# Optimization experiments

Measured on AMD Instinct MI355X. Metric: run time of the kernel, lower is better.

The kernel has to match this reference:

```python
import jax, jax.numpy as jnp
import numpy as np

IMG_SHAPE = (256, 256, 256)


def _rot3(a):
    # Rx @ Ry @ Rz, matching _compute_rotation
    ax, ay, az = a[0], a[1], a[2]
    cx, sx = jnp.cos(ax), jnp.sin(ax)
    cy, sy = jnp.cos(ay), jnp.sin(ay)
    cz, sz = jnp.cos(az), jnp.sin(az)
    one = jnp.ones_like(ax)
    zero = jnp.zeros_like(ax)
    Rx = jnp.stack([jnp.stack([one, zero, zero]),
                    jnp.stack([zero, cx, -sx]),
                    jnp.stack([zero, sx, cx])])
    Ry = jnp.stack([jnp.stack([cy, zero, sy]),
                    jnp.stack([zero, one, zero]),
                    jnp.stack([-sy, zero, cy])])
    Rz = jnp.stack([jnp.stack([cz, -sz, zero]),
                    jnp.stack([sz, cz, zero]),
                    jnp.stack([zero, zero, one])])
    return Rx @ Ry @ Rz


def _rigid4(a, t, cog):
    # T_center_inv @ T_trans @ T_rot @ T_center
    R = _rot3(a)
    Tc = jnp.eye(4, dtype=a.dtype).at[:3, 3].set(-cog)
    Tci = jnp.eye(4, dtype=a.dtype).at[:3, 3].set(cog)
    Tt = jnp.eye(4, dtype=a.dtype).at[:3, 3].set(t)
    Tr = jnp.eye(4, dtype=a.dtype).at[:3, :3].set(R)
    return Tci @ Tt @ Tr @ Tc


def _trilinear(vol, di, dj, dk):
    # fast_3D_interp_torch(mode='linear'): trilinear interp, zero outside bounds
    D, H, W = vol.shape
    ok = (di >= 0) & (di <= D - 1) & (dj >= 0) & (dj <= H - 1) & (dk >= 0) & (dk <= W - 1)
    di = jnp.clip(di, 0.0, D - 1)
    dj = jnp.clip(dj, 0.0, H - 1)
    dk = jnp.clip(dk, 0.0, W - 1)
    fi = jnp.floor(di).astype(jnp.int32)
    fj = jnp.floor(dj).astype(jnp.int32)
    fk = jnp.floor(dk).astype(jnp.int32)
    ci = jnp.clip(fi + 1, 0, D - 1)
    cj = jnp.clip(fj + 1, 0, H - 1)
    ck = jnp.clip(fk + 1, 0, W - 1)
    wi = di - fi
    wj = dj - fj
    wk = dk - fk
    out = (vol[fi, fj, fk] * (1 - wi) * (1 - wj) * (1 - wk)
           + vol[fi, fj, ck] * (1 - wi) * (1 - wj) * wk
           + vol[fi, cj, fk] * (1 - wi) * wj * (1 - wk)
           + vol[fi, cj, ck] * (1 - wi) * wj * wk
           + vol[ci, fj, fk] * wi * (1 - wj) * (1 - wk)
           + vol[ci, fj, ck] * wi * (1 - wj) * wk
           + vol[ci, cj, fk] * wi * wj * (1 - wk)
           + vol[ci, cj, ck] * wi * wj * wk)
    return jnp.where(ok, out, jnp.zeros_like(out))


def setup_inputs() -> dict:
    key = jax.random.key(0)
    k1, k2 = jax.random.split(key)
    image_targ = jax.random.normal(k1, (1, 1) + IMG_SHAPE, dtype=jnp.float32)
    # small rotation so most of the warped grid stays in bounds (angle_factor=1)
    angle = 0.1 * jax.random.normal(k2, (1, 3), dtype=jnp.float32)
    translation = jnp.zeros((1, 3), dtype=jnp.float32)
    v2r = np.eye(4, dtype=np.float32)
    v2r[:3, 3] = -127.5  # center-of-volume RAS origin
    ref_v2r = jnp.asarray(v2r)
    flo_v2r = jnp.asarray(v2r)
    cog = jnp.zeros((3,), dtype=jnp.float32)
    return {"image_targ": image_targ, "angle": angle, "translation": translation,
            "ref_v2r": ref_v2r, "flo_v2r": flo_v2r, "cog": cog}


def reference(image_targ, angle, translation, ref_v2r, flo_v2r, cog):
    # tx_factor = angle_factor = 1 -> params used as-is
    T_rig = jax.vmap(lambda a, t: _rigid4(a, t, cog))(angle, translation)  # [B,4,4]
    T = (jnp.linalg.inv(flo_v2r) @ T_rig[0] @ ref_v2r).astype(jnp.float32)
    D, H, W = image_targ.shape[2:]
    gi, gj, gk = jnp.meshgrid(jnp.arange(D, dtype=jnp.float32),
                              jnp.arange(H, dtype=jnp.float32),
                              jnp.arange(W, dtype=jnp.float32), indexing='ij')
    di = T[0, 0] * gi + T[0, 1] * gj + T[0, 2] * gk + T[0, 3]
    dj = T[1, 0] * gi + T[1, 1] * gj + T[1, 2] * gk + T[1, 3]
    dk = T[2, 0] * gi + T[2, 1] * gj + T[2, 2] * gk + T[2, 3]
    image_reg = _trilinear(image_targ[0, 0], di, dj, dk)
    return image_reg[None, None]
```

## Files before the change

### kernel.cpp

```cpp
#include <hip/hip_runtime.h>
#include <math.h>

#define DD 256
#define HH 256
#define WW 256
#define TI 16
#define TJ 8
#define TK 16
#define LDSF 8192

typedef float f2v __attribute__((ext_vector_type(2)));
typedef f2v __attribute__((aligned(4))) f2u;
typedef float f4v __attribute__((ext_vector_type(4)));
typedef f4v __attribute__((aligned(4))) f4u;

__global__ void compute_T_kernel(const float* __restrict__ angle,
                                 const float* __restrict__ trans,
                                 const float* __restrict__ ref_v2r,
                                 const float* __restrict__ flo_v2r,
                                 const float* __restrict__ cog,
                                 float* __restrict__ Tout ) {
    if (blockIdx.x != 0 || threadIdx.x != 0) return;

    const float ax = angle[0], ay = angle[1], az = angle[2];
    const float cx = cosf(ax), sx = sinf(ax);
    const float cy = cosf(ay), sy = sinf(ay);
    const float cz = cosf(az), sz = sinf(az);

    float R[3][3];
    const float a00 = cy,       a01 = 0.0f, a02 = sy;
    const float a10 = sx * sy,  a11 = cx,   a12 = -sx * cy;
    const float a20 = -cx * sy, a21 = sx,   a22 = cx * cy;
    R[0][0] = a00 * cz + a01 * sz; R[0][1] = -a00 * sz + a01 * cz; R[0][2] = a02;
    R[1][0] = a10 * cz + a11 * sz; R[1][1] = -a10 * sz + a11 * cz; R[1][2] = a12;
    R[2][0] = a20 * cz + a21 * sz; R[2][1] = -a20 * sz + a21 * cz; R[2][2] = a22;

    float Trig[4][4];
    for (int r = 0; r < 4; ++r)
        for (int c = 0; c < 4; ++c)
            Trig[r][c] = (r == c) ? 1.0f : 0.0f;
    for (int r = 0; r < 3; ++r) {
        for (int c = 0; c < 3; ++c) Trig[r][c] = R[r][c];
        Trig[r][3] = cog[r] + trans[r]
                   - (R[r][0] * cog[0] + R[r][1] * cog[1] + R[r][2] * cog[2]);
    }

    float m[16], inv[16];
    for (int q = 0; q < 16; ++q) m[q] = flo_v2r[q];
    inv[0]  =  m[5]*m[10]*m[15] - m[5]*m[11]*m[14] - m[9]*m[6]*m[15]
             + m[9]*m[7]*m[14] + m[13]*m[6]*m[11] - m[13]*m[7]*m[10];
    inv[4]  = -m[4]*m[10]*m[15] + m[4]*m[11]*m[14] + m[8]*m[6]*m[15]
             - m[8]*m[7]*m[14] - m[12]*m[6]*m[11] + m[12]*m[7]*m[10];
    inv[8]  =  m[4]*m[9]*m[15] - m[4]*m[11]*m[13] - m[8]*m[5]*m[15]
             + m[8]*m[7]*m[13] + m[12]*m[5]*m[11] - m[12]*m[7]*m[9];
    inv[12] = -m[4]*m[9]*m[14] + m[4]*m[10]*m[13] + m[8]*m[5]*m[14]
             - m[8]*m[6]*m[13] - m[12]*m[5]*m[10] + m[12]*m[6]*m[9];
    inv[1]  = -m[1]*m[10]*m[15] + m[1]*m[11]*m[14] + m[9]*m[2]*m[15]
             - m[9]*m[3]*m[14] - m[13]*m[2]*m[11] + m[13]*m[3]*m[10];
    inv[5]  =  m[0]*m[10]*m[15] - m[0]*m[11]*m[14] - m[8]*m[2]*m[15]
             + m[8]*m[3]*m[14] + m[12]*m[2]*m[11] - m[12]*m[3]*m[10];
    inv[9]  = -m[0]*m[9]*m[15] + m[0]*m[11]*m[13] + m[8]*m[1]*m[15]
             - m[8]*m[3]*m[13] - m[12]*m[1]*m[11] + m[12]*m[3]*m[9];
    inv[13] =  m[0]*m[9]*m[14] - m[0]*m[10]*m[13] - m[8]*m[1]*m[14]
             + m[8]*m[2]*m[13] + m[12]*m[1]*m[10] - m[12]*m[2]*m[9];
    inv[2]  =  m[1]*m[6]*m[15] - m[1]*m[7]*m[14] - m[5]*m[2]*m[15]
             + m[5]*m[3]*m[14] + m[13]*m[2]*m[7] - m[13]*m[3]*m[6];
    inv[6]  = -m[0]*m[6]*m[15] + m[0]*m[7]*m[14] + m[4]*m[2]*m[15]
             - m[4]*m[3]*m[14] - m[12]*m[2]*m[7] + m[12]*m[3]*m[6];
    inv[10] =  m[0]*m[5]*m[15] - m[0]*m[7]*m[13] - m[4]*m[1]*m[15]
             + m[4]*m[3]*m[13] + m[12]*m[1]*m[7] - m[12]*m[3]*m[5];
    inv[14] = -m[0]*m[5]*m[14] + m[0]*m[6]*m[13] + m[4]*m[1]*m[14]
             - m[4]*m[2]*m[13] - m[12]*m[1]*m[6] + m[12]*m[2]*m[5];
    inv[3]  = -m[1]*m[6]*m[11] + m[1]*m[7]*m[10] + m[5]*m[2]*m[11]
             - m[5]*m[3]*m[10] - m[9]*m[2]*m[7] + m[9]*m[3]*m[6];
    inv[7]  =  m[0]*m[6]*m[11] - m[0]*m[7]*m[10] - m[4]*m[2]*m[11]
             + m[4]*m[3]*m[10] + m[8]*m[2]*m[7] - m[8]*m[3]*m[6];
    inv[11] = -m[0]*m[5]*m[11] + m[0]*m[7]*m[9] + m[4]*m[1]*m[11]
             - m[4]*m[3]*m[9] - m[8]*m[1]*m[7] + m[8]*m[3]*m[5];
    inv[15] =  m[0]*m[5]*m[10] - m[0]*m[6]*m[9] - m[4]*m[1]*m[10]
             + m[4]*m[2]*m[9] + m[8]*m[1]*m[6] - m[8]*m[2]*m[5];
    const float det = m[0]*inv[0] + m[1]*inv[4] + m[2]*inv[8] + m[3]*inv[12];
    const float rdet = 1.0f / det;

    float M1[4][4];
    for (int r = 0; r < 4; ++r)
        for (int c = 0; c < 4; ++c) {
            float s = 0.0f;
            for (int q = 0; q < 4; ++q) s += Trig[r][q] * ref_v2r[q * 4 + c];
            M1[r][c] = s;
        }
    for (int r = 0; r < 3; ++r)
        for (int c = 0; c < 4; ++c) {
            float s = 0.0f;
            for (int q = 0; q < 4; ++q) s += (inv[r * 4 + q] * rdet) * M1[q][c];
            Tout[r * 4 + c] = s;
        }
}

__global__ __launch_bounds__(256) void warp_kernel(
        const float* __restrict__ vol,
        const float* __restrict__ T,
        float* __restrict__ out) {
    const float t0 = T[0],  t1 = T[1],  t2  = T[2],  t3  = T[3];
    const float t4 = T[4],  t5 = T[5],  t6  = T[6],  t7  = T[7];
    const float t8 = T[8],  t9 = T[9],  t10 = T[10], t11 = T[11];

    const int bid = blockIdx.x;
    const int xcd = bid & 7;
    const int n = bid >> 3;
    const int bi = (xcd >> 2) & 1;
    const int bj = (xcd >> 1) & 1;
    const int bk = xcd & 1;
    const int kt = n & 7;
    const int jt = (n >> 3) & 15;
    const int it = n >> 7;

    const int i0 = (bi << 7) + (it << 4);
    const int j0 = (bj << 7) + (jt << 3);
    const int k0 = (bk << 7) + (kt << 4);

    const int tid = threadIdx.x;
    const int kl = tid & 15;
    const int jl = (tid >> 4) & 7;
    const int ihalf = tid >> 7;
    const int j = j0 + jl;
    const int k = k0 + kl;
    const float gj = (float)j, gk = (float)k;
    const int out_base = (i0 << 16) + (j << 8) + k;

    __shared__ float sv[LDSF];

    float mni =  1e30f, mxi = -1e30f;
    float mnj =  1e30f, mxj = -1e30f;
    float mnk =  1e30f, mxk = -1e30f;
#pragma unroll
    for (int c = 0; c < 8; ++c) {
        const float ci_ = (float)(i0 + ((c & 1) ? (TI - 1) : 0));
        const float cj_ = (float)(j0 + ((c & 2) ? (TJ - 1) : 0));
        const float ck_ = (float)(k0 + ((c & 4) ? (TK - 1) : 0));
        const float di = t0 * ci_ + t1 * cj_ + t2  * ck_ + t3;
        const float dj = t4 * ci_ + t5 * cj_ + t6  * ck_ + t7;
        const float dk = t8 * ci_ + t9 * cj_ + t10 * ck_ + t11;
        mni = fminf(mni, di); mxi = fmaxf(mxi, di);
        mnj = fminf(mnj, dj); mxj = fmaxf(mxj, dj);
        mnk = fminf(mnk, dk); mxk = fmaxf(mxk, dk);
    }
    int lo_i = (int)fminf(fmaxf(mni, 0.0f), 255.0f);
    int hi_i = (int)fminf(fmaxf(mxi, 0.0f), 255.0f);
    int lo_j = (int)fminf(fmaxf(mnj, 0.0f), 255.0f);
    int hi_j = (int)fminf(fmaxf(mxj, 0.0f), 255.0f);
    int lo_k = (int)fminf(fmaxf(mnk, 0.0f), 255.0f);
    int hi_k = (int)fminf(fmaxf(mxk, 0.0f), 255.0f);
    lo_i = min(max(lo_i - 1, 0), 252);
    lo_j = min(max(lo_j - 1, 0), 252);
    lo_k = min(max(lo_k - 1, 0), 252);
    hi_i = min(max(hi_i + 2, lo_i + 3), 255);
    hi_j = min(max(hi_j + 2, lo_j + 3), 255);
    hi_k = min(max(hi_k + 2, lo_k + 3), 255);
    const int Si = hi_i - lo_i + 1;
    const int Sj = hi_j - lo_j + 1;
    int Sk  = hi_k - lo_k + 1;
    int SkL = (Sk + 3) & ~3;
    if (lo_k + SkL > 256) {
        lo_k = 256 - SkL;
        Sk = hi_k - lo_k + 1;
        SkL = (Sk + 3) & ~3;
    }
    int Pk = SkL;
    if ((Pk & 7) == 0) Pk += 4;
    const int SjPk = Sj * Pk;
    const bool fits = (Si * SjPk <= LDSF) && (Sj <= 16) && (Sk <= 32);

    if (fits) {
        {
            const int lj  = tid & 15;
            const int c4  = (tid >> 4) & 7;
            const int li0 = tid >> 7;
            const int kk  = c4 << 2;
            if (lj < Sj && kk < SkL) {
                const float* gp = vol + ((lo_i + li0) << 16)
                                      + ((lo_j + lj) << 8) + lo_k + kk;
                float* sp = sv + (li0 * Sj + lj) * Pk + kk;
                int li = li0;
                for (; li + 2 < Si; li += 4) {
                    const f4v a = *(const f4u*)gp;
                    const f4v b = *(const f4u*)(gp + (2 << 16));
                    *(f4u*)sp = a;
                    *(f4u*)(sp + 2 * SjPk) = b;
                    gp += 4 << 16;
                    sp += 4 * SjPk;
                }
                for (; li < Si; li += 2) {
                    *(f4u*)sp = *(const f4u*)gp;
                    gp += 2 << 16;
                    sp += 2 * SjPk;
                }
            }
        }
        __syncthreads();

#pragma unroll
        for (int IT = 0; IT < 2; ++IT) {
            const float gi_ = (float)(i0 + ihalf * 8 + IT * 4);
            float di_ = t0 * gi_ + t1 * gj + t2  * gk + t3;
            float dj_ = t4 * gi_ + t5 * gj + t6  * gk + t7;
            float dk_ = t8 * gi_ + t9 * gj + t10 * gk + t11;
#pragma unroll
            for (int s_ = 0; s_ < 4; ++s_) {
                const float cdi = fminf(fmaxf(di_, 0.0f), (float)(DD - 1));
                const float cdj = fminf(fmaxf(dj_, 0.0f), (float)(HH - 1));
                const float cdk = fminf(fmaxf(dk_, 0.0f), (float)(WW - 1));
                const int fi = (int)cdi;
                const int fj = (int)cdj;
                const int fk = (int)cdk;
                const int ci = min(fi + 1, DD - 1);
                const int cj = min(fj + 1, HH - 1);
                const int pk = min(fk, WW - 2);
                const float wi = cdi - (float)fi;
                const float wj = cdj - (float)fj;
                const float wk = cdk - (float)pk;
                const bool ok_ = (di_ >= 0.0f) & (di_ <= (float)(DD - 1)) &
                                 (dj_ >= 0.0f) & (dj_ <= (float)(HH - 1)) &
                                 (dk_ >= 0.0f) & (dk_ <= (float)(WW - 1));

                const int o_fi = (fi - lo_i) * SjPk;
                const int o_ci = (ci - lo_i) * SjPk;
                const int o_fj = (fj - lo_j) * Pk;
                const int o_cj = (cj - lo_j) * Pk;
                const int pl = pk - lo_k;

                const f2v v0 = *(const f2u*)(sv + o_fi + o_fj + pl);
                const f2v v1 = *(const f2u*)(sv + o_fi + o_cj + pl);
                const f2v v2 = *(const f2u*)(sv + o_ci + o_fj + pl);
                const f2v v3 = *(const f2u*)(sv + o_ci + o_cj + pl);

                const float c00 = v0.x + (v0.y - v0.x) * wk;
                const float c01 = v1.x + (v1.y - v1.x) * wk;
                const float c10 = v2.x + (v2.y - v2.x) * wk;
                const float c11 = v3.x + (v3.y - v3.x) * wk;
                const float c0  = c00 + (c01 - c00) * wj;
                const float c1  = c10 + (c11 - c10) * wj;
                const float val = c0 + (c1 - c0) * wi;

                __builtin_nontemporal_store(ok_ ? val : 0.0f,
                    &out[out_base + ((ihalf * 8 + IT * 4 + s_) << 16)]);

                di_ += t0; dj_ += t4; dk_ += t8;
            }
        }
    } else {
#pragma unroll
        for (int IT = 0; IT < 2; ++IT) {
            const float gi_ = (float)(i0 + ihalf * 8 + IT * 4);
            float di_ = t0 * gi_ + t1 * gj + t2  * gk + t3;
            float dj_ = t4 * gi_ + t5 * gj + t6  * gk + t7;
            float dk_ = t8 * gi_ + t9 * gj + t10 * gk + t11;
#pragma unroll
            for (int s_ = 0; s_ < 4; ++s_) {
                const float cdi = fminf(fmaxf(di_, 0.0f), (float)(DD - 1));
                const float cdj = fminf(fmaxf(dj_, 0.0f), (float)(HH - 1));
                const float cdk = fminf(fmaxf(dk_, 0.0f), (float)(WW - 1));
                const int fi = (int)cdi;
                const int fj = (int)cdj;
                const int fk = (int)cdk;
                const int ci = min(fi + 1, DD - 1);
                const int cj = min(fj + 1, HH - 1);
                const int pk = min(fk, WW - 2);
                const float wi = cdi - (float)fi;
                const float wj = cdj - (float)fj;
                const float wk = cdk - (float)pk;
                const bool ok_ = (di_ >= 0.0f) & (di_ <= (float)(DD - 1)) &
                                 (dj_ >= 0.0f) & (dj_ <= (float)(HH - 1)) &
                                 (dk_ >= 0.0f) & (dk_ <= (float)(WW - 1));

                const int fi_o = fi << 16, ci_o = ci << 16;
                const int fj_o = fj << 8,  cj_o = cj << 8;
                const f2v v0 = *(const f2u*)(vol + (fi_o + fj_o + pk));
                const f2v v1 = *(const f2u*)(vol + (fi_o + cj_o + pk));
                const f2v v2 = *(const f2u*)(vol + (ci_o + fj_o + pk));
                const f2v v3 = *(const f2u*)(vol + (ci_o + cj_o + pk));

                const float c00 = v0.x + (v0.y - v0.x) * wk;
                const float c01 = v1.x + (v1.y - v1.x) * wk;
                const float c10 = v2.x + (v2.y - v2.x) * wk;
                const float c11 = v3.x + (v3.y - v3.x) * wk;
                const float c0  = c00 + (c01 - c00) * wj;
                const float c1  = c10 + (c11 - c10) * wj;
                const float val = c0 + (c1 - c0) * wi;

                __builtin_nontemporal_store(ok_ ? val : 0.0f,
                    &out[out_base + ((ihalf * 8 + IT * 4 + s_) << 16)]);

                di_ += t0; dj_ += t4; dk_ += t8;
            }
        }
    }
}

extern "C" void kernel_launch(void* const* d_in, const int* in_sizes, int n_in,
                              void* d_out, int out_size, void* d_ws, size_t ws_size,
                              hipStream_t stream) {
    const float* image_targ  = (const float*)d_in[0];
    const float* angle       = (const float*)d_in[1];
    const float* translation = (const float*)d_in[2];
    const float* ref_v2r     = (const float*)d_in[3];
    const float* flo_v2r     = (const float*)d_in[4];
    const float* cog         = (const float*)d_in[5];
    float* out = (float*)d_out;
    float* Tws = (float*)d_ws;

    compute_T_kernel<<<1, 64, 0, stream>>>(angle, translation, ref_v2r,
                                           flo_v2r, cog, Tws);
    warp_kernel<<<(DD / TI) * (HH / TJ) * (WW / TK), 256, 0, stream>>>(
        image_targ, Tws, out);
}
```

Measured before the change: 170.4 us.

## Software-pipeline LDS box staging across four i-tiles per persistent block

Each block now handles four consecutive 16-deep i-tiles instead of one, so the grid shrinks to 2048 blocks. The global load of the next tile's source box into registers is overlapped with interpolation from the current LDS box, then written to LDS between barriers. The staging copy is also reworked into a flat, division-free index mapping of eight float4 loads per thread, and the Sk<=32 fit condition is dropped. The aim is to hide global-load latency and amortise block setup. In exchange it adds register pressure for eight float4 staging registers, extra barriers, and fewer blocks to spread across the CUs.

Result: slower. 181.0 us (+6.2%).

```diff
diff --git a/kernel.cpp b/kernel.cpp
--- a/kernel.cpp
+++ b/kernel.cpp
@@ -7,6 +7,7 @@
 #define TI 16
 #define TJ 8
 #define TK 16
+#define NT 4
 #define LDSF 8192
 
 typedef float f2v __attribute__((ext_vector_type(2)));
@@ -97,6 +98,12 @@
         }
 }
 
+struct BoxT {
+    int lo_i, lo_j, lo_k;
+    int Si, Sj, Pk, SkL, SjPk, total;
+    bool fits;
+};
+
 __global__ __launch_bounds__(256) void warp_kernel(
         const float* __restrict__ vol,
         const float* __restrict__ T,
@@ -113,11 +120,11 @@
     const int bk = xcd & 1;
     const int kt = n & 7;
     const int jt = (n >> 3) & 15;
-    const int it = n >> 7;
-
-    const int i0 = (bi << 7) + (it << 4);
-    const int j0 = (bj << 7) + (jt << 3);
-    const int k0 = (bk << 7) + (kt << 4);
+    const int iq = (n >> 7) & 1;
+
+    const int i0q = (bi << 7) + (iq << 6);
+    const int j0  = (bj << 7) + (jt << 3);
+    const int k0  = (bk << 7) + (kt << 4);
 
     const int tid = threadIdx.x;
     const int kl = tid & 15;
@@ -126,82 +133,92 @@
     const int j = j0 + jl;
     const int k = k0 + kl;
     const float gj = (float)j, gk = (float)k;
-    const int out_base = (i0 << 16) + (j << 8) + k;
-
-    __shared__ float sv[LDSF];
-
-    float mni =  1e30f, mxi = -1e30f;
-    float mnj =  1e30f, mxj = -1e30f;
-    float mnk =  1e30f, mxk = -1e30f;
-#pragma unroll
-    for (int c = 0; c < 8; ++c) {
-        const float ci_ = (float)(i0 + ((c & 1) ? (TI - 1) : 0));
-        const float cj_ = (float)(j0 + ((c & 2) ? (TJ - 1) : 0));
-        const float ck_ = (float)(k0 + ((c & 4) ? (TK - 1) : 0));
-        const float di = t0 * ci_ + t1 * cj_ + t2  * ck_ + t3;
-        const float dj = t4 * ci_ + t5 * cj_ + t6  * ck_ + t7;
-        const float dk = t8 * ci_ + t9 * cj_ + t10 * ck_ + t11;
-        mni = fminf(mni, di); mxi = fmaxf(mxi, di);
-        mnj = fminf(mnj, dj); mxj = fmaxf(mxj, dj);
-        mnk = fminf(mnk, dk); mxk = fmaxf(mxk, dk);
-    }
-    int lo_i = (int)fminf(fmaxf(mni, 0.0f), 255.0f);
-    int hi_i = (int)fminf(fmaxf(mxi, 0.0f), 255.0f);
-    int lo_j = (int)fminf(fmaxf(mnj, 0.0f), 255.0f);
-    int hi_j = (int)fminf(fmaxf(mxj, 0.0f), 255.0f);
-    int lo_k = (int)fminf(fmaxf(mnk, 0.0f), 255.0f);
-    int hi_k = (int)fminf(fmaxf(mxk, 0.0f), 255.0f);
-    lo_i = min(max(lo_i - 1, 0), 252);
-    lo_j = min(max(lo_j - 1, 0), 252);
-    lo_k = min(max(lo_k - 1, 0), 252);
-    hi_i = min(max(hi_i + 2, lo_i + 3), 255);
-    hi_j = min(max(hi_j + 2, lo_j + 3), 255);
-    hi_k = min(max(hi_k + 2, lo_k + 3), 255);
-    const int Si = hi_i - lo_i + 1;
-    const int Sj = hi_j - lo_j + 1;
-    int Sk  = hi_k - lo_k + 1;
-    int SkL = (Sk + 3) & ~3;
-    if (lo_k + SkL > 256) {
-        lo_k = 256 - SkL;
-        Sk = hi_k - lo_k + 1;
-        SkL = (Sk + 3) & ~3;
-    }
-    int Pk = SkL;
-    if ((Pk & 7) == 0) Pk += 4;
-    const int SjPk = Sj * Pk;
-    const bool fits = (Si * SjPk <= LDSF) && (Sj <= 16) && (Sk <= 32);
-
-    if (fits) {
-        {
-            const int lj  = tid & 15;
-            const int c4  = (tid >> 4) & 7;
-            const int li0 = tid >> 7;
-            const int kk  = c4 << 2;
-            if (lj < Sj && kk < SkL) {
-                const float* gp = vol + ((lo_i + li0) << 16)
-                                      + ((lo_j + lj) << 8) + lo_k + kk;
-                float* sp = sv + (li0 * Sj + lj) * Pk + kk;
-                int li = li0;
-                for (; li + 2 < Si; li += 4) {
-                    const f4v a = *(const f4u*)gp;
-                    const f4v b = *(const f4u*)(gp + (2 << 16));
-                    *(f4u*)sp = a;
-                    *(f4u*)(sp + 2 * SjPk) = b;
-                    gp += 4 << 16;
-                    sp += 4 * SjPk;
-                }
-                for (; li < Si; li += 2) {
-                    *(f4u*)sp = *(const f4u*)gp;
-                    gp += 2 << 16;
-                    sp += 2 * SjPk;
-                }
-            }
-        }
-        __syncthreads();
-
+
+    __shared__ __align__(16) float sv[LDSF];
+
+    auto mkbox = [&](int i0t) -> BoxT {
+        float mni =  1e30f, mxi = -1e30f;
+        float mnj =  1e30f, mxj = -1e30f;
+        float mnk =  1e30f, mxk = -1e30f;
+#pragma unroll
+        for (int c = 0; c < 8; ++c) {
+            const float ci_ = (float)(i0t + ((c & 1) ? (TI - 1) : 0));
+            const float cj_ = (float)(j0 + ((c & 2) ? (TJ - 1) : 0));
+            const float ck_ = (float)(k0 + ((c & 4) ? (TK - 1) : 0));
+            const float di = t0 * ci_ + t1 * cj_ + t2  * ck_ + t3;
+            const float dj = t4 * ci_ + t5 * cj_ + t6  * ck_ + t7;
+            const float dk = t8 * ci_ + t9 * cj_ + t10 * ck_ + t11;
+            mni = fminf(mni, di); mxi = fmaxf(mxi, di);
+            mnj = fminf(mnj, dj); mxj = fmaxf(mxj, dj);
+            mnk = fminf(mnk, dk); mxk = fmaxf(mxk, dk);
+        }
+        int lo_i = (int)fminf(fmaxf(mni, 0.0f), 255.0f);
+        int hi_i = (int)fminf(fmaxf(mxi, 0.0f), 255.0f);
+        int lo_j = (int)fminf(fmaxf(mnj, 0.0f), 255.0f);
+        int hi_j = (int)fminf(fmaxf(mxj, 0.0f), 255.0f);
+        int lo_k = (int)fminf(fmaxf(mnk, 0.0f), 255.0f);
+        int hi_k = (int)fminf(fmaxf(mxk, 0.0f), 255.0f);
+        lo_i = min(max(lo_i - 1, 0), 252);
+        lo_j = min(max(lo_j - 1, 0), 252);
+        lo_k = min(max(lo_k - 1, 0), 252);
+        hi_i = min(max(hi_i + 2, lo_i + 3), 255);
+        hi_j = min(max(hi_j + 2, lo_j + 3), 255);
+        hi_k = min(max(hi_k + 2, lo_k + 3), 255);
+        BoxT B;
+        B.Si = hi_i - lo_i + 1;
+        B.Sj = hi_j - lo_j + 1;
+        int Sk  = hi_k - lo_k + 1;
+        int SkL = (Sk + 3) & ~3;
+        if (lo_k + SkL > 256) {
+            lo_k = 256 - SkL;
+            Sk = hi_k - lo_k + 1;
+            SkL = (Sk + 3) & ~3;
+        }
+        int Pk = SkL;
+        if ((Pk & 7) == 0) Pk += 4;
+        B.lo_i = lo_i; B.lo_j = lo_j; B.lo_k = lo_k;
+        B.Pk = Pk; B.SkL = SkL;
+        B.SjPk = B.Sj * Pk;
+        B.total = B.Si * B.SjPk;
+        B.fits = (B.total <= LDSF) && (B.Sj <= 16);
+        return B;
+    };
+
+    f4v r[8];
+
+    auto stage_load = [&](const BoxT& B) {
+        const float invPk = 1.0f / (float)B.Pk;
+        const float invSj = 1.0f / (float)B.Sj;
+#pragma unroll
+        for (int q = 0; q < 8; ++q) {
+            int fl = (tid << 2) + (q << 10);
+            fl = min(fl, B.total - 4);
+            const float ff = (float)fl + 0.5f;
+            const int rowid = (int)(ff * invPk);
+            const int kk = fl - rowid * B.Pk;
+            const float fr = (float)rowid + 0.5f;
+            const int li = (int)(fr * invSj);
+            const int lj = rowid - li * B.Sj;
+            const int kkg = min(kk, B.SkL - 4);
+            const float* gp = vol + ((B.lo_i + li) << 16)
+                                  + ((B.lo_j + lj) << 8) + (B.lo_k + kkg);
+            r[q] = *(const f4u*)gp;
+        }
+    };
+
+    auto stage_write = [&]() {
+#pragma unroll
+        for (int q = 0; q < 8; ++q) {
+            const int fl = (tid << 2) + (q << 10);
+            *(f4u*)(sv + fl) = r[q];
+        }
+    };
+
+    auto consume_lds = [&](const BoxT& B, int i0t) {
+        const int ob = (i0t << 16) + (j << 8) + k;
 #pragma unroll
         for (int IT = 0; IT < 2; ++IT) {
-            const float gi_ = (float)(i0 + ihalf * 8 + IT * 4);
+            const float gi_ = (float)(i0t + ihalf * 8 + IT * 4);
             float di_ = t0 * gi_ + t1 * gj + t2  * gk + t3;
             float dj_ = t4 * gi_ + t5 * gj + t6  * gk + t7;
             float dk_ = t8 * gi_ + t9 * gj + t10 * gk + t11;
@@ -223,11 +240,11 @@
                                  (dj_ >= 0.0f) & (dj_ <= (float)(HH - 1)) &
                                  (dk_ >= 0.0f) & (dk_ <= (float)(WW - 1));
 
-                const int o_fi = (fi - lo_i) * SjPk;
-                const int o_ci = (ci - lo_i) * SjPk;
-                const int o_fj = (fj - lo_j) * Pk;
-                const int o_cj = (cj - lo_j) * Pk;
-                const int pl = pk - lo_k;
+                const int o_fi = (fi - B.lo_i) * B.SjPk;
+                const int o_ci = (ci - B.lo_i) * B.SjPk;
+                const int o_fj = (fj - B.lo_j) * B.Pk;
+                const int o_cj = (cj - B.lo_j) * B.Pk;
+                const int pl = pk - B.lo_k;
 
                 const f2v v0 = *(const f2u*)(sv + o_fi + o_fj + pl);
                 const f2v v1 = *(const f2u*)(sv + o_fi + o_cj + pl);
@@ -243,15 +260,18 @@
                 const float val = c0 + (c1 - c0) * wi;
 
                 __builtin_nontemporal_store(ok_ ? val : 0.0f,
-                    &out[out_base + ((ihalf * 8 + IT * 4 + s_) << 16)]);
+                    &out[ob + ((ihalf * 8 + IT * 4 + s_) << 16)]);
 
                 di_ += t0; dj_ += t4; dk_ += t8;
             }
         }
-    } else {
+    };
+
+    auto consume_glob = [&](int i0t) {
+        const int ob = (i0t << 16) + (j << 8) + k;
 #pragma unroll
         for (int IT = 0; IT < 2; ++IT) {
-            const float gi_ = (float)(i0 + ihalf * 8 + IT * 4);
+            const float gi_ = (float)(i0t + ihalf * 8 + IT * 4);
             float di_ = t0 * gi_ + t1 * gj + t2  * gk + t3;
             float dj_ = t4 * gi_ + t5 * gj + t6  * gk + t7;
             float dk_ = t8 * gi_ + t9 * gj + t10 * gk + t11;
@@ -289,10 +309,41 @@
                 const float val = c0 + (c1 - c0) * wi;
 
                 __builtin_nontemporal_store(ok_ ? val : 0.0f,
-                    &out[out_base + ((ihalf * 8 + IT * 4 + s_) << 16)]);
+                    &out[ob + ((ihalf * 8 + IT * 4 + s_) << 16)]);
 
                 di_ += t0; dj_ += t4; dk_ += t8;
             }
+        }
+    };
+
+    BoxT Bc = mkbox(i0q);
+    if (Bc.fits) { stage_load(Bc); stage_write(); }
+    __syncthreads();
+
+#pragma unroll
+    for (int t = 0; t < NT; ++t) {
+        const int i0t = i0q + (t << 4);
+        BoxT Bn;
+        if (t + 1 < NT) {
+            Bn = mkbox(i0q + ((t + 1) << 4));
+            if (Bn.fits) {
+                stage_load(Bn);
+                __builtin_amdgcn_sched_barrier(0);
+            }
+        }
+        if (Bc.fits) consume_lds(Bc, i0t);
+        else         consume_glob(i0t);
+        if (t + 1 < NT) {
+            if (Bn.fits) {
+                __builtin_amdgcn_sched_barrier(0);
+#pragma unroll
+                for (int q = 0; q < 8; ++q) asm volatile("" : "+v"(r[q]));
+                __builtin_amdgcn_sched_barrier(0);
+            }
+            __syncthreads();
+            if (Bn.fits) stage_write();
+            __syncthreads();
+            Bc = Bn;
         }
     }
 }
@@ -311,6 +362,5 @@
 
     compute_T_kernel<<<1, 64, 0, stream>>>(angle, translation, ref_v2r,
                                            flo_v2r, cog, Tws);
-    warp_kernel<<<(DD / TI) * (HH / TJ) * (WW / TK), 256, 0, stream>>>(
-        image_targ, Tws, out);
+    warp_kernel<<<2048, 256, 0, stream>>>(image_targ, Tws, out);
 }
```
